# Kernel optimization log

Hardware: AMD Instinct MI355X
Metric: run time of the kernel (lower is better)

Reference implementation:

```python
import jax, jax.numpy as jnp
import numpy as np

NUM_GRAPHS = 500
BN_EPS = 1e-5


def setup_inputs() -> dict:
    key = jax.random.key(0)
    ks = jax.random.split(key, 16)
    N, E, F, D, L = 100000, 1600000, 128, 128, 3
    x = jax.random.normal(ks[0], (N, F), dtype=jnp.float32)
    edge_index = jax.random.randint(ks[1], (2, E), 0, N)
    batch = jnp.sort(jax.random.randint(ks[2], (N,), 0, NUM_GRAPHS))
    s = 1.0 / np.sqrt(F)
    sd = 1.0 / np.sqrt(D)
    # SAGEConv layer 0: out = lin_l(mean_aggr(x_j)) + lin_r(x)
    sage_Wl = jax.random.uniform(ks[3], (F, D), jnp.float32, -s, s)
    sage_bl = jax.random.uniform(ks[4], (D,), jnp.float32, -s, s)
    sage_Wr = jax.random.uniform(ks[5], (F, D), jnp.float32, -s, s)
    # GINConv layers 1..L-1: nn = Linear(D,D) -> ReLU -> Linear(D,D)
    gin_W1 = jax.random.uniform(ks[6], (L - 1, D, D), jnp.float32, -sd, sd)
    gin_b1 = jax.random.uniform(ks[7], (L - 1, D), jnp.float32, -sd, sd)
    gin_W2 = jax.random.uniform(ks[8], (L - 1, D, D), jnp.float32, -sd, sd)
    gin_b2 = jax.random.uniform(ks[9], (L - 1, D), jnp.float32, -sd, sd)
    bn_gamma = jnp.ones((L, D), dtype=jnp.float32)
    bn_beta = jnp.zeros((L, D), dtype=jnp.float32)
    return {"x": x, "edge_index": edge_index, "batch": batch,
            "sage_Wl": sage_Wl, "sage_bl": sage_bl, "sage_Wr": sage_Wr,
            "gin_W1": gin_W1, "gin_b1": gin_b1, "gin_W2": gin_W2, "gin_b2": gin_b2,
            "bn_gamma": bn_gamma, "bn_beta": bn_beta}


def _batchnorm(h, gamma, beta):
    mu = jnp.mean(h, axis=0)
    var = jnp.var(h, axis=0)  # biased, as torch BN uses for normalization
    return (h - mu) * jax.lax.rsqrt(var + BN_EPS) * gamma + beta


def reference(x, edge_index, batch, sage_Wl, sage_bl, sage_Wr,
              gin_W1, gin_b1, gin_W2, gin_b2, bn_gamma, bn_beta):
    N = x.shape[0]
    src, dst = edge_index[0], edge_index[1]
    L = bn_gamma.shape[0]

    # Layer 0: SAGEConv (mean aggregation, root weight, no bias on lin_r)
    deg = jax.ops.segment_sum(jnp.ones_like(dst, dtype=x.dtype), dst, num_segments=N)
    aggr = jax.ops.segment_sum(x[src], dst, num_segments=N)
    aggr = aggr / jnp.maximum(deg, 1.0)[:, None]
    h = aggr @ sage_Wl + sage_bl + x @ sage_Wr
    h = jax.nn.relu(h)
    h = _batchnorm(h, bn_gamma[0], bn_beta[0])
    xs = [h]

    # Layers 1..L-1: GINConv (eps=0): nn(x + sum_aggr(x_j))
    for i in range(1, L):
        aggr = jax.ops.segment_sum(h[src], dst, num_segments=N)
        t = h + aggr
        t = jax.nn.relu(t @ gin_W1[i - 1] + gin_b1[i - 1])
        t = t @ gin_W2[i - 1] + gin_b2[i - 1]
        h = jax.nn.relu(t)
        h = _batchnorm(h, bn_gamma[i], bn_beta[i])
        xs.append(h)

    # pooling != 'last': concat global_add_pool over every layer
    pooled = jnp.concatenate(
        [jax.ops.segment_sum(xi, batch, num_segments=NUM_GRAPHS) for xi in xs], axis=1)
    node_feats = jnp.concatenate(xs, axis=1)
    return (pooled, node_feats)
```

## Files before the change

### kernel.cpp

```cpp
#include <hip/hip_runtime.h>
#include <hip/hip_bf16.h>


#define BN_EPS 1e-5f
#define EPB 4096

typedef short s8v __attribute__((ext_vector_type(8)));
typedef float f4v __attribute__((ext_vector_type(4)));

__device__ __forceinline__ float bflo(unsigned u) { return __uint_as_float(u << 16); }
__device__ __forceinline__ float bfhi(unsigned u) { return __uint_as_float(u & 0xffff0000u); }
__device__ __forceinline__ unsigned short f2bf(float f) {
    unsigned u = __float_as_uint(f);
    unsigned r = (u + 0x7fffu + ((u >> 16) & 1u)) >> 16;
    return (unsigned short)r;
}
__device__ __forceinline__ unsigned pk2(float a, float b) {
    return (unsigned)f2bf(a) | ((unsigned)f2bf(b) << 16);
}
__device__ __forceinline__ void unpack8(uint4 u, float* v) {
    v[0] = bflo(u.x); v[1] = bfhi(u.x);
    v[2] = bflo(u.y); v[3] = bfhi(u.y);
    v[4] = bflo(u.z); v[5] = bfhi(u.z);
    v[6] = bflo(u.w); v[7] = bfhi(u.w);
}


__global__ __launch_bounds__(256) void k_binA(const int* __restrict__ src,
                                              const int* __restrict__ dst, int E, int NB, int CAP,
                                              int* __restrict__ bcnt,
                                              unsigned long long* __restrict__ ebuf) {
    __shared__ int hist[512], base[512], cur[512];
    const int tid = threadIdx.x;
    const int e0 = blockIdx.x * EPB;
    for (int i = tid; i < 512; i += 256) { hist[i] = 0; cur[i] = 0; }
    __syncthreads();
#pragma unroll
    for (int k = 0; k < EPB / 256; k++) {
        int e = e0 + k * 256 + tid;
        if (e < E) atomicAdd(&hist[dst[e] >> 8], 1);
    }
    __syncthreads();
    for (int b = tid; b < NB; b += 256)
        base[b] = hist[b] ? atomicAdd(&bcnt[b], hist[b]) : 0;
    __syncthreads();
#pragma unroll
    for (int k = 0; k < EPB / 256; k++) {
        int e = e0 + k * 256 + tid;
        if (e < E) {
            int d = dst[e];
            int b = d >> 8;
            int lp = atomicAdd(&cur[b], 1);
            int gp = base[b] + lp;
            if (gp < CAP)
                ebuf[(size_t)b * CAP + gp] = ((unsigned long long)d << 32) | (unsigned)src[e];
        }
    }
}

__global__ __launch_bounds__(256) void k_binB(const unsigned long long* __restrict__ ebuf,
                                              int CAP, const int* __restrict__ bcnt,
                                              int N, int E,
                                              int* __restrict__ rp, int* __restrict__ csr) {
    __shared__ int deg[256], sc[256], cur[256];
    __shared__ int s_cbase;
    const int tid = threadIdx.x;
    const int b = blockIdx.x;
    const int cnt = min(bcnt[b], CAP);

    int partial = 0;
    for (int i = tid; i < b; i += 256) partial += bcnt[i];
    sc[tid] = partial;
    __syncthreads();
    for (int off = 128; off > 0; off >>= 1) {
        if (tid < off) sc[tid] += sc[tid + off];
        __syncthreads();
    }
    if (tid == 0) s_cbase = sc[0];
    __syncthreads();
    const int cbase = s_cbase;

    deg[tid] = 0;
    __syncthreads();
    const unsigned long long* eb = ebuf + (size_t)b * CAP;
    for (int i = tid; i < cnt; i += 256) {
        int d = (int)(eb[i] >> 32);
        atomicAdd(&deg[d & 255], 1);
    }
    __syncthreads();
    int myDeg = deg[tid];
    sc[tid] = myDeg;
    __syncthreads();
    for (int off = 1; off < 256; off <<= 1) {
        int v = (tid >= off) ? sc[tid - off] : 0;
        __syncthreads();
        sc[tid] += v;
        __syncthreads();
    }
    int pos = cbase + sc[tid] - myDeg;
    int node = b * 256 + tid;
    if (node < N) rp[node] = pos;
    cur[tid] = pos;
    __syncthreads();
    for (int i = tid; i < cnt; i += 256) {
        unsigned long long e = eb[i];
        int d = (int)(e >> 32);
        int p = atomicAdd(&cur[d & 255], 1);
        csr[p] = (int)(e & 0xffffffffu);
    }
    if (b == 0 && tid == 0) rp[N] = E;
}


__global__ void k_cvt_bf16(const float* __restrict__ in, uint4* __restrict__ out, int n8) {
    int i = blockIdx.x * 256 + threadIdx.x;
    if (i >= n8) return;
    const float4* p = reinterpret_cast<const float4*>(in) + (size_t)i * 2;
    float4 a = p[0], b = p[1];
    uint4 o;
    o.x = pk2(a.x, a.y); o.y = pk2(a.z, a.w);
    o.z = pk2(b.x, b.y); o.w = pk2(b.z, b.w);
    out[i] = o;
}

__global__ void k_pack_all(const float* __restrict__ sWl, const float* __restrict__ sWr,
                           const float* __restrict__ gW1, const float* __restrict__ gW2,
                           unsigned short* __restrict__ out) {
    int gid = blockIdx.x;
    int wsel = gid >> 6;
    int idx = (gid & 63) * 256 + threadIdx.x;
    const float* W;
    switch (wsel) {
        case 0: W = sWl; break;
        case 1: W = sWr; break;
        case 2: W = gW1; break;
        case 3: W = gW2; break;
        case 4: W = gW1 + 16384; break;
        default: W = gW2 + 16384; break;
    }
    int k = idx >> 7, d = idx & 127;
    float w = W[idx];
    unsigned short h = f2bf(w);
    float hf = __uint_as_float((unsigned)h << 16);
    unsigned short l = f2bf(w - hf);
    int o = (((k >> 3) * 128) + d) * 8 + (k & 7);
    unsigned short* slot = out + (size_t)wsel * 32768;
    slot[o] = h;
    slot[16384 + o] = l;
}

__global__ void k_cvt_h(const float* __restrict__ y,
                        const float* __restrict__ gsumL, const float* __restrict__ gsqL,
                        const float* __restrict__ gamma, const float* __restrict__ beta,
                        float invN, uint4* __restrict__ out, int N) {
    int idx = blockIdx.x * 256 + threadIdx.x;
    if (idx >= N * 16) return;
    int n = idx >> 4, cc = idx & 15;
    float av[8], cv[8];
#pragma unroll
    for (int k = 0; k < 8; k++) {
        int d = cc * 8 + k;
        float mu = gsumL[d] * invN;
        float var = gsqL[d] * invN - mu * mu;
        float rs = rsqrtf(var + BN_EPS);
        float aa = gamma[d] * rs;
        av[k] = aa;
        cv[k] = beta[d] - mu * aa;
    }
    const float* p = y + (size_t)n * 384 + cc * 8;
    float4 x0 = *reinterpret_cast<const float4*>(p);
    float4 x1 = *reinterpret_cast<const float4*>(p + 4);
    uint4 o;
    o.x = pk2(fmaf(x0.x, av[0], cv[0]), fmaf(x0.y, av[1], cv[1]));
    o.y = pk2(fmaf(x0.z, av[2], cv[2]), fmaf(x0.w, av[3], cv[3]));
    o.z = pk2(fmaf(x1.x, av[4], cv[4]), fmaf(x1.y, av[5], cv[5]));
    o.w = pk2(fmaf(x1.z, av[6], cv[6]), fmaf(x1.w, av[7], cv[7]));
    out[(size_t)n * 16 + cc] = o;
}


template <bool SELF, bool MEAN>
__global__ __launch_bounds__(256) void k_aggr(const int* __restrict__ rp,
                                              const int* __restrict__ csr,
                                              const uint4* __restrict__ src,
                                              uint4* __restrict__ out, int N) {
    const int node = blockIdx.x * 4 + (threadIdx.x >> 6);
    if (node >= N) return;
    const int lane = threadIdx.x & 63;
    const int c = lane & 15, grp = lane >> 4;

    float acc[8];
#pragma unroll
    for (int k = 0; k < 8; k++) acc[k] = 0.f;

    const int lo = rp[node], hi = rp[node + 1];
    int j = lo + grp;
    for (; j + 12 < hi; j += 16) {
        int sn0 = csr[j];
        int sn1 = csr[j + 4];
        int sn2 = csr[j + 8];
        int sn3 = csr[j + 12];
        uint4 r0 = src[(size_t)sn0 * 16 + c];
        uint4 r1 = src[(size_t)sn1 * 16 + c];
        uint4 r2 = src[(size_t)sn2 * 16 + c];
        uint4 r3 = src[(size_t)sn3 * 16 + c];
        float v[8];
        unpack8(r0, v);
#pragma unroll
        for (int k = 0; k < 8; k++) acc[k] += v[k];
        unpack8(r1, v);
#pragma unroll
        for (int k = 0; k < 8; k++) acc[k] += v[k];
        unpack8(r2, v);
#pragma unroll
        for (int k = 0; k < 8; k++) acc[k] += v[k];
        unpack8(r3, v);
#pragma unroll
        for (int k = 0; k < 8; k++) acc[k] += v[k];
    }
    for (; j + 4 < hi; j += 8) {
        int sn0 = csr[j];
        int sn1 = csr[j + 4];
        uint4 r0 = src[(size_t)sn0 * 16 + c];
        uint4 r1 = src[(size_t)sn1 * 16 + c];
        float v[8];
        unpack8(r0, v);
#pragma unroll
        for (int k = 0; k < 8; k++) acc[k] += v[k];
        unpack8(r1, v);
#pragma unroll
        for (int k = 0; k < 8; k++) acc[k] += v[k];
    }
    if (j < hi) {
        float v[8];
        unpack8(src[(size_t)csr[j] * 16 + c], v);
#pragma unroll
        for (int k = 0; k < 8; k++) acc[k] += v[k];
    }

#pragma unroll
    for (int k = 0; k < 8; k++) {
        acc[k] += __shfl_xor(acc[k], 16, 64);
        acc[k] += __shfl_xor(acc[k], 32, 64);
    }

    if (grp == 0) {
        if (SELF) {
            float v[8];
            unpack8(src[(size_t)node * 16 + c], v);
#pragma unroll
            for (int k = 0; k < 8; k++) acc[k] += v[k];
        }
        if (MEAN) {
            float inv = 1.0f / fmaxf((float)(hi - lo), 1.0f);
#pragma unroll
            for (int k = 0; k < 8; k++) acc[k] *= inv;
        }
        uint4 o;
        o.x = pk2(acc[0], acc[1]); o.y = pk2(acc[2], acc[3]);
        o.z = pk2(acc[4], acc[5]); o.w = pk2(acc[6], acc[7]);
        out[(size_t)node * 16 + c] = o;
    }
}


#define MFMA_STAGE(Whi, Wlo, B0, B1, ACC)                                          \
    _Pragma("unroll")                                                              \
    for (int ks = 0; ks < 4; ks++) {                                               \
        s8v b0 = __builtin_bit_cast(s8v, B0[ks]);                                  \
        s8v b1 = __builtin_bit_cast(s8v, B1[ks]);                                  \
        _Pragma("unroll")                                                          \
        for (int df = 0; df < 8; df++) {                                           \
            int wi = (ks * 4 + lg) * 128 + df * 16 + l16;                          \
            s8v ah = __builtin_bit_cast(s8v, Whi[wi]);                             \
            s8v al = __builtin_bit_cast(s8v, Wlo[wi]);                             \
            ACC[0][df] = __builtin_amdgcn_mfma_f32_16x16x32_bf16(ah, b0, ACC[0][df], 0, 0, 0); \
            ACC[1][df] = __builtin_amdgcn_mfma_f32_16x16x32_bf16(ah, b1, ACC[1][df], 0, 0, 0); \
            ACC[0][df] = __builtin_amdgcn_mfma_f32_16x16x32_bf16(al, b0, ACC[0][df], 0, 0, 0); \
            ACC[1][df] = __builtin_amdgcn_mfma_f32_16x16x32_bf16(al, b1, ACC[1][df], 0, 0, 0); \
        }                                                                          \
    }

#define STATS_EPILOGUE(OO, V0, V1)                                                 \
    {                                                                              \
        _Pragma("unroll")                                                          \
        for (int df = 0; df < 8; df++) {                                           \
            float s[4], q[4];                                                      \
            _Pragma("unroll")                                                      \
            for (int r = 0; r < 4; r++) {                                          \
                float a0 = V0 ? (&OO[0][df].x)[r] : 0.f;                           \
                float a1 = V1 ? (&OO[1][df].x)[r] : 0.f;                           \
                s[r] = a0 + a1;                                                    \
                q[r] = a0 * a0 + a1 * a1;                                          \
            }                                                                      \
            _Pragma("unroll")                                                      \
            for (int m = 1; m < 16; m <<= 1) {                                     \
                _Pragma("unroll")                                                  \
                for (int r = 0; r < 4; r++) {                                      \
                    s[r] += __shfl_xor(s[r], m, 64);                               \
                    q[r] += __shfl_xor(q[r], m, 64);                               \
                }                                                                  \
            }                                                                      \
            if (l16 == 0) {                                                        \
                _Pragma("unroll")                                                  \
                for (int r = 0; r < 4; r++) {                                      \
                    sred[wid][df * 16 + lg * 4 + r][0] = s[r];                     \
                    sred[wid][df * 16 + lg * 4 + r][1] = q[r];                     \
                }                                                                  \
            }                                                                      \
        }                                                                          \
        __syncthreads();                                                           \
        if (tid < 128) {                                                           \
            float s = sred[0][tid][0] + sred[1][tid][0] + sred[2][tid][0] + sred[3][tid][0]; \
            float q = sred[0][tid][1] + sred[1][tid][1] + sred[2][tid][1] + sred[3][tid][1]; \
            unsafeAtomicAdd(&gsum[tid], s);                                        \
            unsafeAtomicAdd(&gsq[tid], q);                                         \
        }                                                                          \
    }


__global__ __launch_bounds__(256) void k_gemm_sage(
    const uint4* __restrict__ A1, const uint4* __restrict__ A2,
    const uint4* __restrict__ Wfrag,
    const float* __restrict__ bias,
    float* __restrict__ outF, float* __restrict__ gsum, float* __restrict__ gsq,
    int N) {
    __shared__ float sred[4][128][2];
    const int tid = threadIdx.x;
    const int lane = tid & 63, wid = tid >> 6;
    const int nbase = blockIdx.x * 128 + wid * 32;
    const int l16 = lane & 15, lg = lane >> 4;

    f4v acc[2][8];
#pragma unroll
    for (int nf = 0; nf < 2; nf++)
#pragma unroll
        for (int df = 0; df < 8; df++)
            acc[nf][df] = (f4v){0.f, 0.f, 0.f, 0.f};

#pragma unroll
    for (int t = 0; t < 2; t++) {
        const uint4* A = t ? A2 : A1;
        const uint4* Whi = Wfrag + (size_t)t * 4096;
        const uint4* Wlo = Whi + 2048;
        uint4 bvec[2][4];
#pragma unroll
        for (int nf = 0; nf < 2; nf++) {
            const uint4* row = A + (size_t)(nbase + nf * 16 + l16) * 16;
#pragma unroll
            for (int ks = 0; ks < 4; ks++) bvec[nf][ks] = row[ks * 4 + lg];
        }
        MFMA_STAGE(Whi, Wlo, bvec[0], bvec[1], acc)
    }

    const bool v0 = (nbase + l16) < N;
    const bool v1 = (nbase + 16 + l16) < N;
    float4 oo[2][8];
#pragma unroll
    for (int df = 0; df < 8; df++) {
        int d0 = df * 16 + lg * 4;
        const float4 bb = *reinterpret_cast<const float4*>(bias + d0);
#pragma unroll
        for (int nf = 0; nf < 2; nf++) {
            oo[nf][df].x = fmaxf(acc[nf][df][0] + bb.x, 0.f);
            oo[nf][df].y = fmaxf(acc[nf][df][1] + bb.y, 0.f);
            oo[nf][df].z = fmaxf(acc[nf][df][2] + bb.z, 0.f);
            oo[nf][df].w = fmaxf(acc[nf][df][3] + bb.w, 0.f);
        }
    }

    STATS_EPILOGUE(oo, v0, v1)

#pragma unroll
    for (int nf = 0; nf < 2; nf++) {
        int n = nbase + nf * 16 + l16;
        if (n < N) {
#pragma unroll
            for (int df = 0; df < 8; df++)
                *reinterpret_cast<float4*>(outF + (size_t)n * 384 + df * 16 + lg * 4) = oo[nf][df];
        }
    }
}


__global__ __launch_bounds__(256) void k_gemm_gin(
    const uint4* __restrict__ A,
    const uint4* __restrict__ W1f, const uint4* __restrict__ W2f,
    const float* __restrict__ b1, const float* __restrict__ b2,
    float* __restrict__ outF, float* __restrict__ gsum, float* __restrict__ gsq,
    int N) {
    __shared__ uint4 tile[2048];
    __shared__ float sred[4][128][2];
    const int tid = threadIdx.x;
    const int lane = tid & 63, wid = tid >> 6;
    const int nbase = blockIdx.x * 128 + wid * 32;
    const int l16 = lane & 15, lg = lane >> 4;

    f4v acc[2][8];
#pragma unroll
    for (int nf = 0; nf < 2; nf++)
#pragma unroll
        for (int df = 0; df < 8; df++)
            acc[nf][df] = (f4v){0.f, 0.f, 0.f, 0.f};

    {
        const uint4* Whi = W1f;
        const uint4* Wlo = W1f + 2048;
        uint4 bvec[2][4];
#pragma unroll
        for (int nf = 0; nf < 2; nf++) {
            const uint4* row = A + (size_t)(nbase + nf * 16 + l16) * 16;
#pragma unroll
            for (int ks = 0; ks < 4; ks++) bvec[nf][ks] = row[ks * 4 + lg];
        }
        MFMA_STAGE(Whi, Wlo, bvec[0], bvec[1], acc)
    }
#pragma unroll
    for (int df = 0; df < 8; df++) {
        int d0 = df * 16 + lg * 4;
        const float4 bb = *reinterpret_cast<const float4*>(b1 + d0);
#pragma unroll
        for (int nf = 0; nf < 2; nf++) {
            float tx = fmaxf(acc[nf][df][0] + bb.x, 0.f);
            float ty = fmaxf(acc[nf][df][1] + bb.y, 0.f);
            float tz = fmaxf(acc[nf][df][2] + bb.z, 0.f);
            float tw = fmaxf(acc[nf][df][3] + bb.w, 0.f);
            uint2 p;
            p.x = pk2(tx, ty);
            p.y = pk2(tz, tw);
            int row = wid * 32 + nf * 16 + l16;
            int col4 = df * 2 + (lg >> 1);
            int slot = row * 16 + (col4 ^ (row & 15));
            *reinterpret_cast<uint2*>(
                reinterpret_cast<char*>(tile) + (size_t)slot * 16 + (lg & 1) * 8) = p;
        }
    }
    __syncthreads();

#pragma unroll
    for (int nf = 0; nf < 2; nf++)
#pragma unroll
        for (int df = 0; df < 8; df++)
            acc[nf][df] = (f4v){0.f, 0.f, 0.f, 0.f};
    {
        const uint4* Whi = W2f;
        const uint4* Wlo = W2f + 2048;
        uint4 bvec[2][4];
#pragma unroll
        for (int nf = 0; nf < 2; nf++) {
            int row = wid * 32 + nf * 16 + l16;
#pragma unroll
            for (int ks = 0; ks < 4; ks++)
                bvec[nf][ks] = tile[row * 16 + ((ks * 4 + lg) ^ (row & 15))];
        }
        MFMA_STAGE(Whi, Wlo, bvec[0], bvec[1], acc)
    }

    const bool v0 = (nbase + l16) < N;
    const bool v1 = (nbase + 16 + l16) < N;
    float4 oo[2][8];
#pragma unroll
    for (int df = 0; df < 8; df++) {
        int d0 = df * 16 + lg * 4;
        const float4 bb = *reinterpret_cast<const float4*>(b2 + d0);
#pragma unroll
        for (int nf = 0; nf < 2; nf++) {
            oo[nf][df].x = fmaxf(acc[nf][df][0] + bb.x, 0.f);
            oo[nf][df].y = fmaxf(acc[nf][df][1] + bb.y, 0.f);
            oo[nf][df].z = fmaxf(acc[nf][df][2] + bb.z, 0.f);
            oo[nf][df].w = fmaxf(acc[nf][df][3] + bb.w, 0.f);
        }
    }

    STATS_EPILOGUE(oo, v0, v1)

#pragma unroll
    for (int nf = 0; nf < 2; nf++) {
        int n = nbase + nf * 16 + l16;
        if (n < N) {
#pragma unroll
            for (int df = 0; df < 8; df++)
                *reinterpret_cast<float4*>(outF + (size_t)n * 384 + df * 16 + lg * 4) = oo[nf][df];
        }
    }
}


__global__ __launch_bounds__(384) void k_finpool(float* __restrict__ nf,
                                                 const float* __restrict__ gsum,
                                                 const float* __restrict__ gsq,
                                                 const float* __restrict__ gamma,
                                                 const float* __restrict__ beta,
                                                 float invN,
                                                 const int* __restrict__ batch,
                                                 int N, float* __restrict__ pooled) {
    const int d = threadIdx.x;
    float mu = gsum[d] * invN;
    float var = gsq[d] * invN - mu * mu;
    float rs = rsqrtf(var + BN_EPS);
    const float a = gamma[d] * rs;
    const float c = beta[d] - mu * a;

    const int n0 = blockIdx.x * 64;
    const int n1 = min(n0 + 64, N);
    float s = 0.f;
    int curg = batch[n0];
    for (int n = n0; n < n1; n++) {
        int g = batch[n];
        if (g != curg) {
            unsafeAtomicAdd(&pooled[(size_t)curg * 384 + d], s);
            s = 0.f;
            curg = g;
        }
        float v = nf[(size_t)n * 384 + d];
        float h = fmaf(v, a, c);
        nf[(size_t)n * 384 + d] = h;
        s += h;
    }
    unsafeAtomicAdd(&pooled[(size_t)curg * 384 + d], s);
}


extern "C" void kernel_launch(void* const* d_in, const int* in_sizes, int n_in,
                              void* d_out, int out_size, void* d_ws, size_t ws_size,
                              hipStream_t stream) {
    const float* x   = (const float*)d_in[0];
    const int*   ei  = (const int*)d_in[1];
    const int*   bat = (const int*)d_in[2];
    const float* sWl = (const float*)d_in[3];
    const float* sbl = (const float*)d_in[4];
    const float* sWr = (const float*)d_in[5];
    const float* gW1 = (const float*)d_in[6];
    const float* gb1 = (const float*)d_in[7];
    const float* gW2 = (const float*)d_in[8];
    const float* gb2 = (const float*)d_in[9];
    const float* bng = (const float*)d_in[10];
    const float* bnb = (const float*)d_in[11];

    const int N = in_sizes[0] / 128;
    const int E = in_sizes[1] / 2;
    const int G = out_size / 384 - N;
    const int* srcp = ei;
    const int* dstp = ei + E;

    char* w = (char*)d_ws;
    auto alloc = [&](size_t bytes) -> void* {
        void* p = (void*)w;
        w += (bytes + 255) & ~(size_t)255;
        return p;
    };
    const size_t Npad = (size_t)(N + 128);
    int*   rp    = (int*)alloc(((size_t)N + 1) * 4);
    int*   csr   = (int*)alloc((size_t)E * 4);
    char*  zreg  = (char*)alloc(2048 + 2 * 3 * 512);
    int*   bcnt  = (int*)zreg;
    float* gsum  = (float*)(zreg + 2048);
    float* gsq   = gsum + 3 * 128;
    unsigned short* Wp = (unsigned short*)alloc((size_t)6 * 2 * 16384 * 2);
    unsigned short* ab = (unsigned short*)alloc(Npad * 256);
    unsigned short* tb = (unsigned short*)alloc(Npad * 256);

    float* pooled = (float*)d_out;
    float* nf     = pooled + (size_t)G * 384;

    const float invN = 1.0f / (float)N;

    const int NB  = (N + 255) / 256;
    int CAP = ((2 * (E / (NB > 0 ? NB : 1)) + 511) / 512) * 512;
    const long long maxcap = (long long)(Npad * 256) / ((long long)NB * 8);
    if ((long long)CAP > maxcap) CAP = (int)(maxcap & ~511LL);
    unsigned long long* ebuf = (unsigned long long*)ab;

    const int egrid = (E + EPB - 1) / EPB;
    const int agrid = (N + 3) / 4;
    const int ggrid = (N + 127) / 128;
    const int vgrid = (N * 16 + 255) / 256;
    const int fgrid = (N + 63) / 64;

    hipMemsetAsync(zreg, 0, 2048 + 2 * 3 * 512, stream);
    hipMemsetAsync(pooled, 0, (size_t)G * 384 * 4, stream);

    k_binA<<<egrid, 256, 0, stream>>>(srcp, dstp, E, NB, CAP, bcnt, ebuf);
    k_binB<<<NB, 256, 0, stream>>>(ebuf, CAP, bcnt, N, E, rp, csr);

    k_cvt_bf16<<<vgrid, 256, 0, stream>>>(x, (uint4*)tb, N * 16);
    k_pack_all<<<6 * 64, 256, 0, stream>>>(sWl, sWr, gW1, gW2, Wp);

    k_aggr<false, true><<<agrid, 256, 0, stream>>>(rp, csr, (const uint4*)tb, (uint4*)ab, N);
    k_gemm_sage<<<ggrid, 256, 0, stream>>>(
        (const uint4*)ab, (const uint4*)tb, (const uint4*)Wp, sbl, nf, gsum, gsq, N);
    k_cvt_h<<<vgrid, 256, 0, stream>>>(nf, gsum, gsq, bng, bnb, invN, (uint4*)tb, N);

    for (int l = 1; l < 3; l++) {
        const uint4* W1p = (const uint4*)(Wp + (size_t)(2 * l) * 32768);
        const uint4* W2p = (const uint4*)(Wp + (size_t)(2 * l + 1) * 32768);
        const float* b1 = gb1 + (size_t)(l - 1) * 128;
        const float* b2 = gb2 + (size_t)(l - 1) * 128;
        float* nfl = nf + (size_t)l * 128;

        k_aggr<true, false><<<agrid, 256, 0, stream>>>(rp, csr, (const uint4*)tb, (uint4*)ab, N);
        k_gemm_gin<<<ggrid, 256, 0, stream>>>(
            (const uint4*)ab, W1p, W2p, b1, b2, nfl, gsum + l * 128, gsq + l * 128, N);
        if (l < 2)
            k_cvt_h<<<vgrid, 256, 0, stream>>>(nfl, gsum + l * 128, gsq + l * 128,
                                               bng + l * 128, bnb + l * 128, invN,
                                               (uint4*)tb, N);
    }

    k_finpool<<<fgrid, 384, 0, stream>>>(nf, gsum, gsq, bng, bnb, invN, bat, N, pooled);
}
```

Baseline: 561.9 us.

## Fuse per-layer BN normalize, bf16 conversion and pooling; merge prep kernels and memsets

Combines the weight packing, the input bf16 conversion and the two memsets into a single prep launch. The per-layer BN-apply/bf16 conversion and the final normalize-and-pool pass are merged into one per-layer kernel that normalizes node features in place, accumulates the graph pooling, and writes the bf16 copy for the next layer. This removes a full re-read of the 384-wide feature array at the end and several launches. The cost is that the bf16 writes become 2-byte per-thread scalar stores, and each pooling launch now uses only 128 threads per block.

```diff
diff --git a/kernel.cpp b/kernel.cpp
--- a/kernel.cpp
+++ b/kernel.cpp
@@ -112,70 +112,51 @@
 }
 
 
-__global__ void k_cvt_bf16(const float* __restrict__ in, uint4* __restrict__ out, int n8) {
-    int i = blockIdx.x * 256 + threadIdx.x;
-    if (i >= n8) return;
-    const float4* p = reinterpret_cast<const float4*>(in) + (size_t)i * 2;
-    float4 a = p[0], b = p[1];
-    uint4 o;
-    o.x = pk2(a.x, a.y); o.y = pk2(a.z, a.w);
-    o.z = pk2(b.x, b.y); o.w = pk2(b.z, b.w);
-    out[i] = o;
-}
-
-__global__ void k_pack_all(const float* __restrict__ sWl, const float* __restrict__ sWr,
-                           const float* __restrict__ gW1, const float* __restrict__ gW2,
-                           unsigned short* __restrict__ out) {
-    int gid = blockIdx.x;
-    int wsel = gid >> 6;
-    int idx = (gid & 63) * 256 + threadIdx.x;
-    const float* W;
-    switch (wsel) {
-        case 0: W = sWl; break;
-        case 1: W = sWr; break;
-        case 2: W = gW1; break;
-        case 3: W = gW2; break;
-        case 4: W = gW1 + 16384; break;
-        default: W = gW2 + 16384; break;
-    }
-    int k = idx >> 7, d = idx & 127;
-    float w = W[idx];
-    unsigned short h = f2bf(w);
-    float hf = __uint_as_float((unsigned)h << 16);
-    unsigned short l = f2bf(w - hf);
-    int o = (((k >> 3) * 128) + d) * 8 + (k & 7);
-    unsigned short* slot = out + (size_t)wsel * 32768;
-    slot[o] = h;
-    slot[16384 + o] = l;
-}
-
-__global__ void k_cvt_h(const float* __restrict__ y,
-                        const float* __restrict__ gsumL, const float* __restrict__ gsqL,
-                        const float* __restrict__ gamma, const float* __restrict__ beta,
-                        float invN, uint4* __restrict__ out, int N) {
-    int idx = blockIdx.x * 256 + threadIdx.x;
-    if (idx >= N * 16) return;
-    int n = idx >> 4, cc = idx & 15;
-    float av[8], cv[8];
-#pragma unroll
-    for (int k = 0; k < 8; k++) {
-        int d = cc * 8 + k;
-        float mu = gsumL[d] * invN;
-        float var = gsqL[d] * invN - mu * mu;
-        float rs = rsqrtf(var + BN_EPS);
-        float aa = gamma[d] * rs;
-        av[k] = aa;
-        cv[k] = beta[d] - mu * aa;
-    }
-    const float* p = y + (size_t)n * 384 + cc * 8;
-    float4 x0 = *reinterpret_cast<const float4*>(p);
-    float4 x1 = *reinterpret_cast<const float4*>(p + 4);
-    uint4 o;
-    o.x = pk2(fmaf(x0.x, av[0], cv[0]), fmaf(x0.y, av[1], cv[1]));
-    o.y = pk2(fmaf(x0.z, av[2], cv[2]), fmaf(x0.w, av[3], cv[3]));
-    o.z = pk2(fmaf(x1.x, av[4], cv[4]), fmaf(x1.y, av[5], cv[5]));
-    o.w = pk2(fmaf(x1.z, av[6], cv[6]), fmaf(x1.w, av[7], cv[7]));
-    out[(size_t)n * 16 + cc] = o;
+__global__ __launch_bounds__(256) void k_prep(
+    const float* __restrict__ sWl, const float* __restrict__ sWr,
+    const float* __restrict__ gW1, const float* __restrict__ gW2,
+    unsigned short* __restrict__ Wp,
+    const float* __restrict__ x, uint4* __restrict__ tb, int n16,
+    uint4* __restrict__ pool4, int npool4, int zpb,
+    uint4* __restrict__ zreg4, int nzreg4) {
+    const int b = blockIdx.x;
+    const int tid = threadIdx.x;
+    if (b < 384) {
+        int wsel = b >> 6;
+        int idx = (b & 63) * 256 + tid;
+        const float* W;
+        switch (wsel) {
+            case 0: W = sWl; break;
+            case 1: W = sWr; break;
+            case 2: W = gW1; break;
+            case 3: W = gW2; break;
+            case 4: W = gW1 + 16384; break;
+            default: W = gW2 + 16384; break;
+        }
+        int k = idx >> 7, d = idx & 127;
+        float w = W[idx];
+        unsigned short h = f2bf(w);
+        float hf = __uint_as_float((unsigned)h << 16);
+        unsigned short l = f2bf(w - hf);
+        int o = (((k >> 3) * 128) + d) * 8 + (k & 7);
+        unsigned short* slot = Wp + (size_t)wsel * 32768;
+        slot[o] = h;
+        slot[16384 + o] = l;
+    } else if (b < 384 + zpb) {
+        int i = (b - 384) * 256 + tid;
+        if (i < npool4) pool4[i] = make_uint4(0, 0, 0, 0);
+    } else if (b == 384 + zpb) {
+        for (int i = tid; i < nzreg4; i += 256) zreg4[i] = make_uint4(0, 0, 0, 0);
+    } else {
+        int i = (b - 385 - zpb) * 256 + tid;
+        if (i >= n16) return;
+        const float4* p = reinterpret_cast<const float4*>(x) + (size_t)i * 2;
+        float4 a = p[0], bb = p[1];
+        uint4 o;
+        o.x = pk2(a.x, a.y); o.y = pk2(a.z, a.w);
+        o.z = pk2(bb.x, bb.y); o.w = pk2(bb.z, bb.w);
+        tb[i] = o;
+    }
 }
 
 
@@ -486,20 +467,19 @@
 }
 
 
-__global__ __launch_bounds__(384) void k_finpool(float* __restrict__ nf,
-                                                 const float* __restrict__ gsum,
-                                                 const float* __restrict__ gsq,
-                                                 const float* __restrict__ gamma,
-                                                 const float* __restrict__ beta,
-                                                 float invN,
-                                                 const int* __restrict__ batch,
-                                                 int N, float* __restrict__ pooled) {
+__global__ __launch_bounds__(128) void k_normpool(
+    float* __restrict__ nfl,
+    const float* __restrict__ gsumL, const float* __restrict__ gsqL,
+    const float* __restrict__ gammaL, const float* __restrict__ betaL,
+    float invN, const int* __restrict__ batch, int N,
+    float* __restrict__ pooledL,
+    unsigned short* __restrict__ tab) {
     const int d = threadIdx.x;
-    float mu = gsum[d] * invN;
-    float var = gsq[d] * invN - mu * mu;
+    float mu = gsumL[d] * invN;
+    float var = gsqL[d] * invN - mu * mu;
     float rs = rsqrtf(var + BN_EPS);
-    const float a = gamma[d] * rs;
-    const float c = beta[d] - mu * a;
+    const float a = gammaL[d] * rs;
+    const float c = betaL[d] - mu * a;
 
     const int n0 = blockIdx.x * 64;
     const int n1 = min(n0 + 64, N);
@@ -508,16 +488,17 @@
     for (int n = n0; n < n1; n++) {
         int g = batch[n];
         if (g != curg) {
-            unsafeAtomicAdd(&pooled[(size_t)curg * 384 + d], s);
+            unsafeAtomicAdd(&pooledL[(size_t)curg * 384 + d], s);
             s = 0.f;
             curg = g;
         }
-        float v = nf[(size_t)n * 384 + d];
+        float v = nfl[(size_t)n * 384 + d];
         float h = fmaf(v, a, c);
-        nf[(size_t)n * 384 + d] = h;
+        nfl[(size_t)n * 384 + d] = h;
         s += h;
-    }
-    unsafeAtomicAdd(&pooled[(size_t)curg * 384 + d], s);
+        if (tab) tab[(size_t)n * 128 + d] = f2bf(h);
+    }
+    unsafeAtomicAdd(&pooledL[(size_t)curg * 384 + d], s);
 }
 
 
@@ -574,22 +555,26 @@
     const int egrid = (E + EPB - 1) / EPB;
     const int agrid = (N + 3) / 4;
     const int ggrid = (N + 127) / 128;
-    const int vgrid = (N * 16 + 255) / 256;
-    const int fgrid = (N + 63) / 64;
-
-    hipMemsetAsync(zreg, 0, 2048 + 2 * 3 * 512, stream);
-    hipMemsetAsync(pooled, 0, (size_t)G * 384 * 4, stream);
-
+    const int pgrid = (N + 63) / 64;
+
+    const int npool4 = G * 96;
+    const int zpb    = (npool4 + 255) / 256;
+    const int nzreg4 = (2048 + 2 * 3 * 512) / 16;
+    const int cvtb   = (N * 16 + 255) / 256;
+    const int prepgrid = 384 + zpb + 1 + cvtb;
+
+    k_prep<<<prepgrid, 256, 0, stream>>>(sWl, sWr, gW1, gW2, Wp,
+                                         x, (uint4*)tb, N * 16,
+                                         (uint4*)pooled, npool4, zpb,
+                                         (uint4*)zreg, nzreg4);
     k_binA<<<egrid, 256, 0, stream>>>(srcp, dstp, E, NB, CAP, bcnt, ebuf);
     k_binB<<<NB, 256, 0, stream>>>(ebuf, CAP, bcnt, N, E, rp, csr);
-
-    k_cvt_bf16<<<vgrid, 256, 0, stream>>>(x, (uint4*)tb, N * 16);
-    k_pack_all<<<6 * 64, 256, 0, stream>>>(sWl, sWr, gW1, gW2, Wp);
 
     k_aggr<false, true><<<agrid, 256, 0, stream>>>(rp, csr, (const uint4*)tb, (uint4*)ab, N);
     k_gemm_sage<<<ggrid, 256, 0, stream>>>(
         (const uint4*)ab, (const uint4*)tb, (const uint4*)Wp, sbl, nf, gsum, gsq, N);
-    k_cvt_h<<<vgrid, 256, 0, stream>>>(nf, gsum, gsq, bng, bnb, invN, (uint4*)tb, N);
+    k_normpool<<<pgrid, 128, 0, stream>>>(nf, gsum, gsq, bng, bnb, invN, bat, N,
+                                          pooled, tb);
 
     for (int l = 1; l < 3; l++) {
         const uint4* W1p = (const uint4*)(Wp + (size_t)(2 * l) * 32768);
@@ -601,11 +586,9 @@
         k_aggr<true, false><<<agrid, 256, 0, stream>>>(rp, csr, (const uint4*)tb, (uint4*)ab, N);
         k_gemm_gin<<<ggrid, 256, 0, stream>>>(
             (const uint4*)ab, W1p, W2p, b1, b2, nfl, gsum + l * 128, gsq + l * 128, N);
-        if (l < 2)
-            k_cvt_h<<<vgrid, 256, 0, stream>>>(nfl, gsum + l * 128, gsq + l * 128,
-                                               bng + l * 128, bnb + l * 128, invN,
-                                               (uint4*)tb, N);
-    }
-
-    k_finpool<<<fgrid, 384, 0, stream>>>(nf, gsum, gsq, bng, bnb, invN, bat, N, pooled);
-}
+        k_normpool<<<pgrid, 128, 0, stream>>>(nfl, gsum + l * 128, gsq + l * 128,
+                                              bng + l * 128, bnb + l * 128, invN, bat, N,
+                                              pooled + (size_t)l * 128,
+                                              (l < 2) ? tb : nullptr);
+    }
+}
```

Measured after the change: 565.5 us. About the same (+0.6%).
